# Kernel optimization log

Hardware: AMD Instinct MI355X
Metric: run time of the kernel (lower is better)

Reference implementation:

```python
import jax, jax.numpy as jnp
import numpy as np
import math

EMBED_DIM = 512
D_K = 64
D_V = 64
B, S = 4, 4096


def setup_inputs() -> dict:
    key = jax.random.key(0)
    ks = jax.random.split(key, 9)
    s = 1.0 / math.sqrt(EMBED_DIM)
    return {
        "query_in": jax.random.normal(ks[0], (B, S, EMBED_DIM), jnp.float32),
        "key_in": jax.random.normal(ks[1], (B, S, EMBED_DIM), jnp.float32),
        "value_in": jax.random.normal(ks[2], (B, S, EMBED_DIM), jnp.float32),
        "Wq": jax.random.normal(ks[3], (EMBED_DIM, D_K), jnp.float32) * s,
        "bq": jnp.zeros((D_K,), jnp.float32),
        "Wk": jax.random.normal(ks[4], (EMBED_DIM, D_K), jnp.float32) * s,
        "bk": jnp.zeros((D_K,), jnp.float32),
        "Wv": jax.random.normal(ks[5], (EMBED_DIM, D_V), jnp.float32) * s,
        "bv": jnp.zeros((D_V,), jnp.float32),
    }


def reference(query_in, key_in, value_in, Wq, bq, Wk, bk, Wv, bv):
    # Linear projections (value computed for faithfulness; unused by the
    # truncated forward, which returns pre-softmax scaled scores)
    q = query_in @ Wq + bq            # [B,S,d_k]
    k = key_in @ Wk + bk              # [B,S,d_k]
    v = value_in @ Wv + bv            # [B,S,d_v] (unused downstream)
    # scaled dot-product scores: Q K^T / sqrt(d_k)  -> [B,S,S]
    scores = jnp.einsum("bqd,bkd->bqk", q, k) / math.sqrt(D_K)
    return scores
```

## Files before the change

### kernel.cpp

```cpp
#include <hip/hip_runtime.h>
#include <hip/hip_bf16.h>

constexpr int Bn = 4;
constexpr int S  = 4096;
constexpr int E  = 512;
constexpr int DK = 64;
constexpr int LDS_STRIDE = DK + 8;

typedef __attribute__((ext_vector_type(8))) short   bf16x8;
typedef __attribute__((ext_vector_type(4))) float   f32x4;

__device__ __forceinline__ unsigned short f2bf(float f) {
    unsigned x = __builtin_bit_cast(unsigned, f);
    unsigned r = x + 0x7FFFu + ((x >> 16) & 1u);
    return (unsigned short)(r >> 16);
}

__device__ __forceinline__ bf16x8 load8_f2bf(const float* __restrict__ p) {
    f32x4 a = *(const f32x4*)p;
    f32x4 b = *(const f32x4*)(p + 4);
    bf16x8 o;
    o[0] = (short)f2bf(a[0]); o[1] = (short)f2bf(a[1]);
    o[2] = (short)f2bf(a[2]); o[3] = (short)f2bf(a[3]);
    o[4] = (short)f2bf(b[0]); o[5] = (short)f2bf(b[1]);
    o[6] = (short)f2bf(b[2]); o[7] = (short)f2bf(b[3]);
    return o;
}

__global__ __launch_bounds__(256) void wt_kernel(const float* __restrict__ Wq,
                                                 const float* __restrict__ Wk,
                                                 unsigned short* __restrict__ Wt) {
    int idx = blockIdx.x * 256 + threadIdx.x;
    const float* W = blockIdx.y ? Wk : Wq;
    int n = idx >> 9;
    int k = idx & 511;
    Wt[blockIdx.y * (DK * E) + idx] = f2bf(W[k * DK + n]);
}

__global__ __launch_bounds__(256) void proj_kernel(const float* __restrict__ Xq,
                                                   const float* __restrict__ Xk,
                                                   const unsigned short* __restrict__ Wt,
                                                   const float* __restrict__ bq,
                                                   const float* __restrict__ bk,
                                                   unsigned short* __restrict__ Qp,
                                                   unsigned short* __restrict__ Kp) {
    const float*          X    = blockIdx.y ? Xk : Xq;
    const unsigned short* Wtm  = Wt + (size_t)blockIdx.y * DK * E;
    const float*          bias = blockIdx.y ? bk : bq;
    unsigned short*       P    = blockIdx.y ? Kp : Qp;

    __shared__ unsigned short xs[128][LDS_STRIDE];

    const int tid  = threadIdx.x;
    const int wave = tid >> 6;
    const int lane = tid & 63;
    const int quad = lane >> 4;
    const int l16  = lane & 15;
    const long row0 = (long)blockIdx.x * 128;

    f32x4 acc[2][4];
#pragma unroll
    for (int rt = 0; rt < 2; ++rt)
#pragma unroll
        for (int ct = 0; ct < 4; ++ct) acc[rt][ct] = (f32x4){0.f, 0.f, 0.f, 0.f};

    for (int k0 = 0; k0 < E; k0 += 64) {
        __syncthreads();
#pragma unroll
        for (int c = tid; c < 1024; c += 256) {
            int r  = c >> 3;
            int kc = (c & 7) * 8;
            *(bf16x8*)&xs[r][kc] = load8_f2bf(&X[(row0 + r) * E + k0 + kc]);
        }
        __syncthreads();

        bf16x8 bfrag[2][4];
#pragma unroll
        for (int kc = 0; kc < 2; ++kc)
#pragma unroll
            for (int ct = 0; ct < 4; ++ct)
                bfrag[kc][ct] = *(const bf16x8*)&Wtm[(size_t)(ct * 16 + l16) * E + k0 + kc * 32 + quad * 8];

#pragma unroll
        for (int rt = 0; rt < 2; ++rt) {
#pragma unroll
            for (int kc = 0; kc < 2; ++kc) {
                bf16x8 afrag = *(const bf16x8*)&xs[wave * 32 + rt * 16 + l16][kc * 32 + quad * 8];
#pragma unroll
                for (int ct = 0; ct < 4; ++ct)
                    acc[rt][ct] = __builtin_amdgcn_mfma_f32_16x16x32_bf16(afrag, bfrag[kc][ct], acc[rt][ct], 0, 0, 0);
            }
        }
    }

#pragma unroll
    for (int ct = 0; ct < 4; ++ct) {
        float bv = bias[ct * 16 + l16];
#pragma unroll
        for (int rt = 0; rt < 2; ++rt) {
#pragma unroll
            for (int r = 0; r < 4; ++r) {
                long row = row0 + wave * 32 + rt * 16 + quad * 4 + r;
                P[row * DK + ct * 16 + l16] = f2bf(acc[rt][ct][r] + bv);
            }
        }
    }
}

__global__ __launch_bounds__(256) void score_kernel(const unsigned short* __restrict__ Q,
                                                    const unsigned short* __restrict__ K,
                                                    float* __restrict__ out) {
    __shared__ unsigned short qs[128][LDS_STRIDE];
    __shared__ unsigned short ks[128][LDS_STRIDE];

    const int tid  = threadIdx.x;
    const int wave = tid >> 6;
    const int lane = tid & 63;
    const int quad = lane >> 4;
    const int l16  = lane & 15;

    const int  b     = blockIdx.z;
    const long qrow0 = (long)blockIdx.y * 128;
    const long krow0 = (long)blockIdx.x * 128;
    const unsigned short* Qb = Q + (size_t)b * S * DK;
    const unsigned short* Kb = K + (size_t)b * S * DK;

#pragma unroll
    for (int c = tid; c < 1024; c += 256) {
        int r  = c >> 3;
        int kc = (c & 7) * 8;
        *(bf16x8*)&qs[r][kc] = *(const bf16x8*)&Qb[(qrow0 + r) * DK + kc];
        *(bf16x8*)&ks[r][kc] = *(const bf16x8*)&Kb[(krow0 + r) * DK + kc];
    }
    __syncthreads();

    const int wr = (wave >> 1) * 64;
    const int wc = (wave & 1) * 64;

    bf16x8 afrag[4][2], bfrag[4][2];
#pragma unroll
    for (int rt = 0; rt < 4; ++rt)
#pragma unroll
        for (int kc = 0; kc < 2; ++kc)
            afrag[rt][kc] = *(const bf16x8*)&qs[wr + rt * 16 + l16][kc * 32 + quad * 8];
#pragma unroll
    for (int ct = 0; ct < 4; ++ct)
#pragma unroll
        for (int kc = 0; kc < 2; ++kc)
            bfrag[ct][kc] = *(const bf16x8*)&ks[wc + ct * 16 + l16][kc * 32 + quad * 8];

    f32x4 acc[4][4];
#pragma unroll
    for (int rt = 0; rt < 4; ++rt)
#pragma unroll
        for (int ct = 0; ct < 4; ++ct) acc[rt][ct] = (f32x4){0.f, 0.f, 0.f, 0.f};

#pragma unroll
    for (int rt = 0; rt < 4; ++rt)
#pragma unroll
        for (int ct = 0; ct < 4; ++ct)
#pragma unroll
            for (int kc = 0; kc < 2; ++kc)
                acc[rt][ct] = __builtin_amdgcn_mfma_f32_16x16x32_bf16(afrag[rt][kc], bfrag[ct][kc], acc[rt][ct], 0, 0, 0);

    float* ob = out + (size_t)b * S * S;
#pragma unroll
    for (int rt = 0; rt < 4; ++rt) {
#pragma unroll
        for (int ct = 0; ct < 4; ++ct) {
#pragma unroll
            for (int r = 0; r < 4; ++r) {
                long row = qrow0 + wr + rt * 16 + quad * 4 + r;
                long col = krow0 + wc + ct * 16 + l16;
                ob[row * S + col] = acc[rt][ct][r] * 0.125f;
            }
        }
    }
}

extern "C" void kernel_launch(void* const* d_in, const int* in_sizes, int n_in,
                              void* d_out, int out_size, void* d_ws, size_t ws_size,
                              hipStream_t stream) {
    (void)in_sizes; (void)n_in; (void)out_size; (void)ws_size;

    const float* query = (const float*)d_in[0];
    const float* key   = (const float*)d_in[1];
    const float* Wq    = (const float*)d_in[3];
    const float* bq    = (const float*)d_in[4];
    const float* Wk    = (const float*)d_in[5];
    const float* bk    = (const float*)d_in[6];

    unsigned short* ws = (unsigned short*)d_ws;
    unsigned short* Wt = ws;
    unsigned short* Qp = ws + 2 * DK * E;
    unsigned short* Kp = Qp + (size_t)Bn * S * DK;

    float* scores = (float*)d_out;

    wt_kernel<<<dim3(128, 2), 256, 0, stream>>>(Wq, Wk, Wt);
    proj_kernel<<<dim3(Bn * S / 128, 2), 256, 0, stream>>>(query, key, Wt, bq, bk, Qp, Kp);
    score_kernel<<<dim3(S / 128, S / 128, Bn), 256, 0, stream>>>(Qp, Kp, scores);
}
```

Baseline: 363.6 us.

## Stage score tiles through LDS for vectorized stores; shrink projection tiles

The score kernel now gives each wave a 32x128 strip instead of a 64x64 tile. It writes the scaled accumulators into a per-wave LDS buffer that reuses the Q/K staging memory, then stores full 16-byte vectors to global memory row by row. This replaces scattered 4-byte stores and targets the write bandwidth of the 256MB output. The projection kernel moves to 32-row blocks with each wave owning a 16x32 output tile, which gives four times more blocks for better occupancy at the cost of reloading weight fragments more often.

```diff
diff --git a/kernel.cpp b/kernel.cpp
--- a/kernel.cpp
+++ b/kernel.cpp
@@ -1,11 +1,10 @@
 #include <hip/hip_runtime.h>
-#include <hip/hip_bf16.h>
 
 constexpr int Bn = 4;
 constexpr int S  = 4096;
 constexpr int E  = 512;
 constexpr int DK = 64;
-constexpr int LDS_STRIDE = DK + 8;
+constexpr int XS_STRIDE = DK + 8;
 
 typedef __attribute__((ext_vector_type(8))) short   bf16x8;
 typedef __attribute__((ext_vector_type(4))) float   f32x4;
@@ -49,60 +48,53 @@
     const float*          bias = blockIdx.y ? bk : bq;
     unsigned short*       P    = blockIdx.y ? Kp : Qp;
 
-    __shared__ unsigned short xs[128][LDS_STRIDE];
+    __shared__ unsigned short xs[32][XS_STRIDE];
 
     const int tid  = threadIdx.x;
     const int wave = tid >> 6;
     const int lane = tid & 63;
     const int quad = lane >> 4;
     const int l16  = lane & 15;
-    const long row0 = (long)blockIdx.x * 128;
-
-    f32x4 acc[2][4];
-#pragma unroll
-    for (int rt = 0; rt < 2; ++rt)
-#pragma unroll
-        for (int ct = 0; ct < 4; ++ct) acc[rt][ct] = (f32x4){0.f, 0.f, 0.f, 0.f};
+    const long row0 = (long)blockIdx.x * 32;
+
+    const int wrt = (wave & 1) * 16;
+    const int wct = (wave >> 1) * 32;
+
+    const int sr = tid >> 3;
+    const int sk = (tid & 7) * 8;
+    const float* xsrc = &X[(row0 + sr) * E + sk];
+
+    f32x4 acc[2];
+    acc[0] = (f32x4){0.f, 0.f, 0.f, 0.f};
+    acc[1] = (f32x4){0.f, 0.f, 0.f, 0.f};
 
     for (int k0 = 0; k0 < E; k0 += 64) {
         __syncthreads();
-#pragma unroll
-        for (int c = tid; c < 1024; c += 256) {
-            int r  = c >> 3;
-            int kc = (c & 7) * 8;
-            *(bf16x8*)&xs[r][kc] = load8_f2bf(&X[(row0 + r) * E + k0 + kc]);
+        *(bf16x8*)&xs[sr][sk] = load8_f2bf(xsrc + k0);
+        __syncthreads();
+
+        bf16x8 bfrag[2][2];
+#pragma unroll
+        for (int kc = 0; kc < 2; ++kc)
+#pragma unroll
+            for (int ct = 0; ct < 2; ++ct)
+                bfrag[kc][ct] = *(const bf16x8*)&Wtm[(size_t)(wct + ct * 16 + l16) * E + k0 + kc * 32 + quad * 8];
+
+#pragma unroll
+        for (int kc = 0; kc < 2; ++kc) {
+            bf16x8 af = *(const bf16x8*)&xs[wrt + l16][kc * 32 + quad * 8];
+            acc[0] = __builtin_amdgcn_mfma_f32_16x16x32_bf16(af, bfrag[kc][0], acc[0], 0, 0, 0);
+            acc[1] = __builtin_amdgcn_mfma_f32_16x16x32_bf16(af, bfrag[kc][1], acc[1], 0, 0, 0);
         }
-        __syncthreads();
-
-        bf16x8 bfrag[2][4];
-#pragma unroll
-        for (int kc = 0; kc < 2; ++kc)
-#pragma unroll
-            for (int ct = 0; ct < 4; ++ct)
-                bfrag[kc][ct] = *(const bf16x8*)&Wtm[(size_t)(ct * 16 + l16) * E + k0 + kc * 32 + quad * 8];
-
-#pragma unroll
-        for (int rt = 0; rt < 2; ++rt) {
-#pragma unroll
-            for (int kc = 0; kc < 2; ++kc) {
-                bf16x8 afrag = *(const bf16x8*)&xs[wave * 32 + rt * 16 + l16][kc * 32 + quad * 8];
-#pragma unroll
-                for (int ct = 0; ct < 4; ++ct)
-                    acc[rt][ct] = __builtin_amdgcn_mfma_f32_16x16x32_bf16(afrag, bfrag[kc][ct], acc[rt][ct], 0, 0, 0);
-            }
-        }
-    }
-
-#pragma unroll
-    for (int ct = 0; ct < 4; ++ct) {
-        float bv = bias[ct * 16 + l16];
-#pragma unroll
-        for (int rt = 0; rt < 2; ++rt) {
-#pragma unroll
-            for (int r = 0; r < 4; ++r) {
-                long row = row0 + wave * 32 + rt * 16 + quad * 4 + r;
-                P[row * DK + ct * 16 + l16] = f2bf(acc[rt][ct][r] + bv);
-            }
+    }
+
+#pragma unroll
+    for (int ct = 0; ct < 2; ++ct) {
+        float bv = bias[wct + ct * 16 + l16];
+#pragma unroll
+        for (int r = 0; r < 4; ++r) {
+            long row = row0 + wrt + quad * 4 + r;
+            P[row * DK + wct + ct * 16 + l16] = f2bf(acc[ct][r] + bv);
         }
     }
 }
@@ -110,8 +102,9 @@
 __global__ __launch_bounds__(256) void score_kernel(const unsigned short* __restrict__ Q,
                                                     const unsigned short* __restrict__ K,
                                                     float* __restrict__ out) {
-    __shared__ unsigned short qs[128][LDS_STRIDE];
-    __shared__ unsigned short ks[128][LDS_STRIDE];
+    __shared__ __align__(16) char smraw[2 * 128 * XS_STRIDE * 2];
+    unsigned short (*qs)[XS_STRIDE] = (unsigned short(*)[XS_STRIDE])smraw;
+    unsigned short (*ks)[XS_STRIDE] = (unsigned short(*)[XS_STRIDE])(smraw + 128 * XS_STRIDE * 2);
 
     const int tid  = threadIdx.x;
     const int wave = tid >> 6;
@@ -134,47 +127,57 @@
     }
     __syncthreads();
 
-    const int wr = (wave >> 1) * 64;
-    const int wc = (wave & 1) * 64;
-
-    bf16x8 afrag[4][2], bfrag[4][2];
-#pragma unroll
-    for (int rt = 0; rt < 4; ++rt)
+    const int wr = wave * 32;
+
+    bf16x8 afrag[2][2];
+#pragma unroll
+    for (int rt = 0; rt < 2; ++rt)
 #pragma unroll
         for (int kc = 0; kc < 2; ++kc)
             afrag[rt][kc] = *(const bf16x8*)&qs[wr + rt * 16 + l16][kc * 32 + quad * 8];
-#pragma unroll
-    for (int ct = 0; ct < 4; ++ct)
-#pragma unroll
-        for (int kc = 0; kc < 2; ++kc)
-            bfrag[ct][kc] = *(const bf16x8*)&ks[wc + ct * 16 + l16][kc * 32 + quad * 8];
-
-    f32x4 acc[4][4];
-#pragma unroll
-    for (int rt = 0; rt < 4; ++rt)
-#pragma unroll
-        for (int ct = 0; ct < 4; ++ct) acc[rt][ct] = (f32x4){0.f, 0.f, 0.f, 0.f};
-
-#pragma unroll
-    for (int rt = 0; rt < 4; ++rt)
-#pragma unroll
-        for (int ct = 0; ct < 4; ++ct)
-#pragma unroll
-            for (int kc = 0; kc < 2; ++kc)
-                acc[rt][ct] = __builtin_amdgcn_mfma_f32_16x16x32_bf16(afrag[rt][kc], bfrag[ct][kc], acc[rt][ct], 0, 0, 0);
+
+    f32x4 acc[2][8];
+#pragma unroll
+    for (int rt = 0; rt < 2; ++rt)
+#pragma unroll
+        for (int ct = 0; ct < 8; ++ct) acc[rt][ct] = (f32x4){0.f, 0.f, 0.f, 0.f};
+
+#pragma unroll
+    for (int ct = 0; ct < 8; ++ct) {
+        bf16x8 b0 = *(const bf16x8*)&ks[ct * 16 + l16][quad * 8];
+        bf16x8 b1 = *(const bf16x8*)&ks[ct * 16 + l16][32 + quad * 8];
+#pragma unroll
+        for (int rt = 0; rt < 2; ++rt) {
+            acc[rt][ct] = __builtin_amdgcn_mfma_f32_16x16x32_bf16(afrag[rt][0], b0, acc[rt][ct], 0, 0, 0);
+            acc[rt][ct] = __builtin_amdgcn_mfma_f32_16x16x32_bf16(afrag[rt][1], b1, acc[rt][ct], 0, 0, 0);
+        }
+    }
+
+    __syncthreads();
+
+    float (*wbuf)[132] = (float(*)[132])(smraw + (size_t)wave * (16 * 132 * 4));
 
     float* ob = out + (size_t)b * S * S;
-#pragma unroll
-    for (int rt = 0; rt < 4; ++rt) {
-#pragma unroll
-        for (int ct = 0; ct < 4; ++ct) {
-#pragma unroll
-            for (int r = 0; r < 4; ++r) {
-                long row = qrow0 + wr + rt * 16 + quad * 4 + r;
-                long col = krow0 + wc + ct * 16 + l16;
-                ob[row * S + col] = acc[rt][ct][r] * 0.125f;
+    const int rrow = lane >> 3;
+    const int rcol = (lane & 7) * 4;
+
+#pragma unroll
+    for (int rt = 0; rt < 2; ++rt) {
+#pragma unroll
+        for (int ct = 0; ct < 8; ++ct)
+#pragma unroll
+            for (int r = 0; r < 4; ++r)
+                wbuf[quad * 4 + r][ct * 16 + l16] = acc[rt][ct][r] * 0.125f;
+
+#pragma unroll
+        for (int jr = 0; jr < 2; ++jr)
+#pragma unroll
+            for (int jc = 0; jc < 4; ++jc) {
+                int rr = jr * 8 + rrow;
+                int cc = jc * 32 + rcol;
+                f32x4 v = *(const f32x4*)&wbuf[rr][cc];
+                *(f32x4*)&ob[(qrow0 + wr + rt * 16 + rr) * S + krow0 + cc] = v;
             }
-        }
     }
 }
 
@@ -198,6 +201,6 @@
     float* scores = (float*)d_out;
 
     wt_kernel<<<dim3(128, 2), 256, 0, stream>>>(Wq, Wk, Wt);
-    proj_kernel<<<dim3(Bn * S / 128, 2), 256, 0, stream>>>(query, key, Wt, bq, bk, Qp, Kp);
+    proj_kernel<<<dim3(Bn * S / 32, 2), 256, 0, stream>>>(query, key, Wt, bq, bk, Qp, Kp);
     score_kernel<<<dim3(S / 128, S / 128, Bn), 256, 0, stream>>>(Qp, Kp, scores);
 }
```

Result: faster. 352.2 us (-3.1%).
